# Kernel optimization log

Measured on AMD Instinct MI355X. Metric: run time of the kernel, lower is better.

Reference implementation:

```python
import jax, jax.numpy as jnp
import numpy as np

B, IN_F, OUT_F = 524288, 128, 128


def setup_inputs() -> dict:
    key = jax.random.key(0)
    k_x, k_wp, k_wn, k_b = jax.random.split(key, 4)
    x = jax.random.normal(k_x, (B, IN_F), dtype=jnp.float32)
    # params initialized uniform(-0.1, 0.1) as in the torch module
    weight_p = jax.random.uniform(k_wp, (OUT_F, IN_F), minval=-0.1, maxval=0.1, dtype=jnp.float32)
    weight_n = jax.random.uniform(k_wn, (OUT_F, IN_F), minval=-0.1, maxval=0.1, dtype=jnp.float32)
    bias = jax.random.uniform(k_b, (OUT_F,), minval=-0.1, maxval=0.1, dtype=jnp.float32)
    return {"x": x, "weight_p": weight_p, "weight_n": weight_n, "bias": bias}


def reference(x, weight_p, weight_n, bias):
    # ternarize: sign with >=0 -> +1 (matches torch.where(w >= 0, +1, -1))
    one = jnp.float32(1.0)
    wp = jnp.where(weight_p >= 0, one, -one)
    wn = jnp.where(weight_n >= 0, one, -one)
    # effective weight in {-1, 0, +1}
    w = (wp - wn) * jnp.float32(0.5)  # [out, in]
    out = x @ w.T + bias[None, :]      # [B, out]
    return out
```

## Files before the change

kernel.cpp:

```cpp
#include <hip/hip_runtime.h>
#include <hip/hip_bf16.h>


typedef short short8 __attribute__((ext_vector_type(8)));
typedef float f32x4 __attribute__((ext_vector_type(4)));
typedef float f32x8 __attribute__((ext_vector_type(8)));

__device__ __forceinline__ short f2bf(float f) {
  unsigned u = __builtin_bit_cast(unsigned, f);
  unsigned r = u + 0x7fffu + ((u >> 16) & 1u);
  return (short)(r >> 16);
}

__global__ void ternarize_kernel(const float* __restrict__ wp,
                                 const float* __restrict__ wn,
                                 short* __restrict__ wt, int n) {
  int i = blockIdx.x * blockDim.x + threadIdx.x;
  if (i < n) {
    float p = wp[i];
    float q = wn[i];
    float v = 0.5f * ((p >= 0.f ? 1.f : -1.f) - (q >= 0.f ? 1.f : -1.f));
    wt[i] = f2bf(v);
  }
}

__launch_bounds__(256, 2)
__global__ void stl_gemm_kernel(const float* __restrict__ x,
                                const short* __restrict__ wt,
                                const float* __restrict__ bias,
                                float* __restrict__ out) {
  constexpr int IN_F = 128;
  constexpr int OUT_F = 128;
  const int wave = threadIdx.x >> 6;
  const int lane = threadIdx.x & 63;
  const int r = lane & 15;
  const int g = lane >> 4;
  const long row0 = (long)blockIdx.x * 128 + wave * 32;

  f32x8 xv[4][2];
#pragma unroll
  for (int kk = 0; kk < 4; ++kk)
#pragma unroll
    for (int m = 0; m < 2; ++m)
      xv[kk][m] = *(const f32x8*)(x + (row0 + m * 16 + r) * IN_F + kk * 32 + g * 8);

  f32x4 acc[2][8] = {};

#pragma unroll
  for (int kk = 0; kk < 4; ++kk) {
    const int k0 = kk * 32 + g * 8;
    short8 bx[2];
#pragma unroll
    for (int m = 0; m < 2; ++m)
#pragma unroll
      for (int j = 0; j < 8; ++j) bx[m][j] = f2bf(xv[kk][m][j]);
#pragma unroll
    for (int c = 0; c < 8; ++c) {
      short8 aw = *(const short8*)(wt + (c * 16 + r) * IN_F + k0);
#pragma unroll
      for (int m = 0; m < 2; ++m)
        acc[m][c] =
            __builtin_amdgcn_mfma_f32_16x16x32_bf16(aw, bx[m], acc[m][c], 0, 0, 0);
    }
  }

#pragma unroll
  for (int c = 0; c < 8; ++c) {
    const f32x4 bv = *(const f32x4*)(bias + c * 16 + g * 4);
#pragma unroll
    for (int m = 0; m < 2; ++m) {
      f32x4 v = acc[m][c] + bv;
      *(f32x4*)(out + (row0 + m * 16 + r) * OUT_F + c * 16 + g * 4) = v;
    }
  }
}

extern "C" void kernel_launch(void* const* d_in, const int* in_sizes, int n_in,
                              void* d_out, int out_size, void* d_ws, size_t ws_size,
                              hipStream_t stream) {
  const float* x    = (const float*)d_in[0];
  const float* wp   = (const float*)d_in[1];
  const float* wn   = (const float*)d_in[2];
  const float* bias = (const float*)d_in[3];
  float* out = (float*)d_out;
  short* wt = (short*)d_ws;

  ternarize_kernel<<<64, 256, 0, stream>>>(wp, wn, wt, 128 * 128);

  stl_gemm_kernel<<<4096, 256, 0, stream>>>(x, wt, bias, out);
}
```

Measured before the change: 470.4 us.

## Pre-swizzle ternary weights into MFMA fragment order and stage via LDS

```diff
diff --git a/kernel.cpp b/kernel.cpp
--- a/kernel.cpp
+++ b/kernel.cpp
@@ -12,43 +12,64 @@
   return (short)(r >> 16);
 }
 
-__global__ void ternarize_kernel(const float* __restrict__ wp,
-                                 const float* __restrict__ wn,
-                                 short* __restrict__ wt, int n) {
-  int i = blockIdx.x * blockDim.x + threadIdx.x;
-  if (i < n) {
-    float p = wp[i];
-    float q = wn[i];
-    float v = 0.5f * ((p >= 0.f ? 1.f : -1.f) - (q >= 0.f ? 1.f : -1.f));
-    wt[i] = f2bf(v);
+__global__ void ternarize_frag_kernel(const float* __restrict__ wp,
+                                      const float* __restrict__ wn,
+                                      short8* __restrict__ wfrag) {
+  const int tid = blockIdx.x * blockDim.x + threadIdx.x;
+  const int lane = tid & 63;
+  const int chunk = tid >> 6;
+  const int kk = chunk >> 3, c = chunk & 7;
+  const int r = lane & 15, g = lane >> 4;
+  const int outcol = c * 16 + r;
+  const int k0 = kk * 32 + g * 8;
+  const float* p = wp + outcol * 128 + k0;
+  const float* q = wn + outcol * 128 + k0;
+  short8 v;
+#pragma unroll
+  for (int j = 0; j < 8; ++j) {
+    float s = 0.5f * ((p[j] >= 0.f ? 1.f : -1.f) - (q[j] >= 0.f ? 1.f : -1.f));
+    v[j] = f2bf(s);
   }
+  wfrag[tid] = v;
 }
 
 __launch_bounds__(256, 2)
 __global__ void stl_gemm_kernel(const float* __restrict__ x,
-                                const short* __restrict__ wt,
+                                const short8* __restrict__ wfrag,
                                 const float* __restrict__ bias,
                                 float* __restrict__ out) {
   constexpr int IN_F = 128;
   constexpr int OUT_F = 128;
-  const int wave = threadIdx.x >> 6;
-  const int lane = threadIdx.x & 63;
+  __shared__ short8 wlds[2048];
+  const int tid = threadIdx.x;
+  const int wave = tid >> 6;
+  const int lane = tid & 63;
   const int r = lane & 15;
   const int g = lane >> 4;
   const long row0 = (long)blockIdx.x * 128 + wave * 32;
+
+#pragma unroll
+  for (int i = 0; i < 8; ++i) {
+    const int chunk = i * 256 + tid;
+    __builtin_amdgcn_global_load_lds(
+        (const __attribute__((address_space(1))) void*)(wfrag + chunk),
+        (__attribute__((address_space(3))) void*)(wlds + chunk),
+        16, 0, 0);
+  }
 
   f32x8 xv[4][2];
 #pragma unroll
   for (int kk = 0; kk < 4; ++kk)
 #pragma unroll
     for (int m = 0; m < 2; ++m)
-      xv[kk][m] = *(const f32x8*)(x + (row0 + m * 16 + r) * IN_F + kk * 32 + g * 8);
+      xv[kk][m] =
+          *(const f32x8*)(x + (row0 + m * 16 + r) * IN_F + kk * 32 + g * 8);
+  __builtin_amdgcn_sched_barrier(0);
+  __syncthreads();
 
   f32x4 acc[2][8] = {};
-
 #pragma unroll
   for (int kk = 0; kk < 4; ++kk) {
-    const int k0 = kk * 32 + g * 8;
     short8 bx[2];
 #pragma unroll
     for (int m = 0; m < 2; ++m)
@@ -56,7 +77,7 @@
       for (int j = 0; j < 8; ++j) bx[m][j] = f2bf(xv[kk][m][j]);
 #pragma unroll
     for (int c = 0; c < 8; ++c) {
-      short8 aw = *(const short8*)(wt + (c * 16 + r) * IN_F + k0);
+      const short8 aw = wlds[(kk * 8 + c) * 64 + lane];
 #pragma unroll
       for (int m = 0; m < 2; ++m)
         acc[m][c] =
@@ -83,9 +104,9 @@
   const float* wn   = (const float*)d_in[2];
   const float* bias = (const float*)d_in[3];
   float* out = (float*)d_out;
-  short* wt = (short*)d_ws;
+  short8* wfrag = (short8*)d_ws;
 
-  ternarize_kernel<<<64, 256, 0, stream>>>(wp, wn, wt, 128 * 128);
+  ternarize_frag_kernel<<<8, 256, 0, stream>>>(wp, wn, wfrag);
 
-  stl_gemm_kernel<<<4096, 256, 0, stream>>>(x, wt, bias, out);
+  stl_gemm_kernel<<<4096, 256, 0, stream>>>(x, wfrag, bias, out);
 }
```

New measurement: 455.6 us. 1.03x faster.
